# Kernel optimization log

Measured on AMD Instinct MI355X. Metric: run time of the kernel, lower is better.

Reference implementation:

```python
import jax, jax.numpy as jnp
import numpy as np

HEADS = 8
TOK = 4  # num_query_tokens
EPS = 1e-5


def _ln(x, w, b):
    mu = jnp.mean(x, -1, keepdims=True)
    v = jnp.var(x, -1, keepdims=True)
    return (x - mu) / jnp.sqrt(v + EPS) * w + b


def _inorm(x):
    # InstanceNorm3d(affine=False): normalize per (B,C) over spatial dims
    mu = jnp.mean(x, (2, 3, 4), keepdims=True)
    v = jnp.var(x, (2, 3, 4), keepdims=True)
    return (x - mu) / jnp.sqrt(v + EPS)


def _conv3(x, w, b):
    y = jax.lax.conv_general_dilated(x, w, (1, 1, 1), 'SAME',
                                     dimension_numbers=('NCDHW', 'OIDHW', 'NCDHW'))
    return y + b[None, :, None, None, None]


def setup_inputs() -> dict:
    key = jax.random.key(0)
    ks = jax.random.split(key, 8)
    B, C, D, H, W = 4, 320, 16, 32, 32
    CLI = 320
    QD = C * TOK  # 1280
    s = 0.02
    return {
        'img_feat': jax.random.normal(ks[0], (B, C, D, H, W), jnp.float32),
        'cli_feat': jax.random.normal(ks[1], (B, CLI), jnp.float32),
        'Wq': jax.random.normal(ks[2], (QD, CLI), jnp.float32) * s,
        'bq': jnp.zeros((QD,), jnp.float32),
        'lnq_w': jnp.ones((QD,), jnp.float32),
        'lnq_b': jnp.zeros((QD,), jnp.float32),
        'Wk': jax.random.normal(ks[3], (C, C), jnp.float32) * s,
        'bk': jnp.zeros((C,), jnp.float32),
        'Wv': jax.random.normal(ks[4], (C, C), jnp.float32) * s,
        'bv': jnp.zeros((C,), jnp.float32),
        'Wo': jax.random.normal(ks[5], (C, QD), jnp.float32) * s,
        'bo': jnp.zeros((C,), jnp.float32),
        'lno_w': jnp.ones((C,), jnp.float32),
        'lno_b': jnp.zeros((C,), jnp.float32),
        'Wf1': jax.random.normal(ks[6], (C, 2 * C, 3, 3, 3), jnp.float32) * s,
        'bf1': jnp.zeros((C,), jnp.float32),
        'Wf2': jax.random.normal(ks[7], (C, C, 3, 3, 3), jnp.float32) * s,
        'bf2': jnp.zeros((C,), jnp.float32),
    }


def reference(img_feat, cli_feat, Wq, bq, lnq_w, lnq_b, Wk, bk, Wv, bv,
              Wo, bo, lno_w, lno_b, Wf1, bf1, Wf2, bf2):
    B, C, D, H, W = img_feat.shape
    S = D * H * W
    hd = C // HEADS
    scale = hd ** -0.5
    # clinical features -> 4 query tokens per head: [B, heads, head_dim, TOK]
    q = _ln(cli_feat @ Wq.T + bq, lnq_w, lnq_b).reshape(B, HEADS, hd, TOK)
    # 1x1x1 convs == per-position linear over channels
    x = img_feat.reshape(B, C, S)
    k = (jnp.einsum('oc,bcs->bos', Wk, x) + bk[None, :, None]).reshape(B, HEADS, hd, S)
    v = (jnp.einsum('oc,bcs->bos', Wv, x) + bv[None, :, None]).reshape(B, HEADS, hd, S)
    # [B, heads, TOK, S] scores -> softmax over spatial
    attn = jax.nn.softmax(jnp.einsum('bhdt,bhds->bhts', q, k) * scale, axis=-1)
    # value @ attn^T -> [B, heads, head_dim, TOK], flatten like torch .view(B,-1)
    o = jnp.einsum('bhds,bhts->bhdt', v, attn).reshape(B, HEADS * hd * TOK)
    o = _ln(o @ Wo.T + bo, lno_w, lno_b)  # [B, C]
    bcast = jnp.broadcast_to(o[:, :, None, None, None], (B, C, D, H, W))
    fused = jnp.concatenate([img_feat, bcast], axis=1)  # [B, 2C, D, H, W]
    h = jax.nn.gelu(_inorm(_conv3(fused, Wf1, bf1)), approximate=False)
    h = _inorm(_conv3(h, Wf2, bf2))
    return h + img_feat
```

## Files before the change

### kernel.cpp

```cpp
#include <hip/hip_runtime.h>
#include <hip/hip_bf16.h>
#include <math.h>

typedef unsigned short u16;

#define DEV static __device__ __forceinline__

DEV float bfu(u16 u) { union { unsigned int i; float f; } v; v.i = ((unsigned int)u) << 16; return v.f; }
DEV u16 fbu(float f) { __hip_bfloat16 h = __float2bfloat16(f); return *reinterpret_cast<u16*>(&h); }

template <typename T> struct ModeOf;
template <> struct ModeOf<u16>   { static constexpr int v = 0; };
template <> struct ModeOf<float> { static constexpr int v = 1; };
template <typename T> DEV float ld(const void* p, size_t i);
template <> DEV float ld<u16>(const void* p, size_t i)   { return bfu(((const u16*)p)[i]); }
template <> DEV float ld<float>(const void* p, size_t i) { return ((const float*)p)[i]; }

template <typename T> DEV float4 ld4(const void* p, size_t i);
template <> DEV float4 ld4<u16>(const void* p, size_t i) {
    ushort4 v = *reinterpret_cast<const ushort4*>((const u16*)p + i);
    return make_float4(bfu(v.x), bfu(v.y), bfu(v.z), bfu(v.w));
}
template <> DEV float4 ld4<float>(const void* p, size_t i) {
    return *reinterpret_cast<const float4*>((const float*)p + i);
}

#define NB 4
#define NC 320
#define ND 16
#define NH 32
#define NW 32
#define NS 16384
#define NHD 40
#define NQD 1280
#define NR 32
#define NTOK 4
#define OUT_N (NB*NC*NS)
#define EPSV 1e-5f
#define SCALE 0.15811388300841898f

#define YKS 8
#define YCH (NS / YKS)

#define CSL 32
#define NSL 10
#define HALO_D 4
#define HALO_H 6
#define PIXW 34
#define NPIX (HALO_D*HALO_H*PIXW)
#define PACKN (27*10*20*64*8)

typedef __attribute__((ext_vector_type(8))) short bf16x8;
typedef __attribute__((ext_vector_type(4))) float f32x4;

DEV int swz4(int p) { return (p + (p >> 2)) & 3; }

DEV float blk_sum(float v, float* red) {
    __syncthreads();
#pragma unroll
    for (int o = 32; o > 0; o >>= 1) v += __shfl_down(v, o, 64);
    int wv = threadIdx.x >> 6, ln = threadIdx.x & 63;
    if (ln == 0) red[wv] = v;
    __syncthreads();
    return red[0] + red[1] + red[2] + red[3];
}
DEV float blk_max(float v, float* red) {
    __syncthreads();
#pragma unroll
    for (int o = 32; o > 0; o >>= 1) v = fmaxf(v, __shfl_down(v, o, 64));
    int wv = threadIdx.x >> 6, ln = threadIdx.x & 63;
    if (ln == 0) red[wv] = v;
    __syncthreads();
    return fmaxf(fmaxf(red[0], red[1]), fmaxf(red[2], red[3]));
}

__global__ void detect_kernel(const u16* __restrict__ lnqw, int* __restrict__ flag) {
    if (threadIdx.x == 0) flag[0] = (lnqw[0] == 0x3F80) ? 0 : 1;
}

template <typename T>
__global__ __launch_bounds__(256) void q_kernel(const int* __restrict__ flag,
        const void* __restrict__ cli, const void* __restrict__ Wq, const void* __restrict__ bq,
        const void* __restrict__ lnw, const void* __restrict__ lnb, float* __restrict__ qout) {
    if (*flag != ModeOf<T>::v) return;
    int b = blockIdx.x, tid = threadIdx.x;
    __shared__ float cl[NC];
    __shared__ float red[8];
    for (int i = tid; i < NC; i += 256) cl[i] = ld<T>(cli, b * NC + i);
    __syncthreads();
    float loc[5];
    float s1 = 0.f, s2 = 0.f;
#pragma unroll
    for (int k = 0; k < 5; ++k) {
        int j = tid + k * 256;
        float a = ld<T>(bq, j);
        size_t wr = (size_t)j * NC;
        for (int c = 0; c < NC; ++c) a += cl[c] * ld<T>(Wq, wr + c);
        loc[k] = a; s1 += a; s2 += a * a;
    }
    s1 = blk_sum(s1, red);
    s2 = blk_sum(s2, red);
    float mu = s1 / (float)NQD;
    float var = fmaxf(s2 / (float)NQD - mu * mu, 0.f);
    float rs = rsqrtf(var + EPSV);
#pragma unroll
    for (int k = 0; k < 5; ++k) {
        int j = tid + k * 256;
        qout[(size_t)b * NQD + j] = (loc[k] - mu) * rs * ld<T>(lnw, j) + ld<T>(lnb, j);
    }
}

template <typename T>
__global__ __launch_bounds__(256) void qw_kernel(const int* __restrict__ flag,
        const float* __restrict__ q, const void* __restrict__ Wk, const void* __restrict__ bk,
        float* __restrict__ qW, float* __restrict__ qb) {
    if (*flag != ModeOf<T>::v) return;
    int gid = blockIdx.x * 256 + threadIdx.x;
    if (gid < NB * NR * NC) {
        int c = gid % NC;
        int r = (gid / NC) % NR;
        int b = gid / (NC * NR);
        int h = r >> 2, t = r & 3;
        float a = 0.f;
        const float* qb_ = q + (size_t)b * NQD;
        for (int d = 0; d < NHD; ++d)
            a += qb_[(h * NHD + d) * NTOK + t] * ld<T>(Wk, (size_t)(h * NHD + d) * NC + c);
        qW[gid] = a;
    }
    if (gid < NB * NR) {
        int r = gid & 31, b = gid >> 5;
        int h = r >> 2, t = r & 3;
        float a = 0.f;
        const float* qb_ = q + (size_t)b * NQD;
        for (int d = 0; d < NHD; ++d)
            a += qb_[(h * NHD + d) * NTOK + t] * ld<T>(bk, h * NHD + d);
        qb[gid] = a;
    }
}

template <typename T>
__global__ __launch_bounds__(256) void scores_kernel(const int* __restrict__ flag,
        const void* __restrict__ img, const float* __restrict__ qW, const float* __restrict__ qb,
        float* __restrict__ attn) {
    if (*flag != ModeOf<T>::v) return;
    int b = blockIdx.y;
    int s = blockIdx.x * 256 + threadIdx.x;
    __shared__ __align__(16) float qWl[NR * NC];
    for (int i = threadIdx.x; i < NR * NC; i += 256) qWl[i] = qW[(size_t)b * NR * NC + i];
    __syncthreads();
    float acc[NR];
#pragma unroll
    for (int r = 0; r < NR; ++r) acc[r] = 0.f;
    size_t xb = (size_t)b * NC * NS + s;
    for (int c0 = 0; c0 < NC; c0 += 4) {
        float x0 = ld<T>(img, xb + ((size_t)(c0 + 0) << 14));
        float x1 = ld<T>(img, xb + ((size_t)(c0 + 1) << 14));
        float x2 = ld<T>(img, xb + ((size_t)(c0 + 2) << 14));
        float x3 = ld<T>(img, xb + ((size_t)(c0 + 3) << 14));
#pragma unroll
        for (int r = 0; r < NR; ++r) {
            const float4 qv = *reinterpret_cast<const float4*>(&qWl[r * NC + c0]);
            acc[r] += qv.x * x0 + qv.y * x1 + qv.z * x2 + qv.w * x3;
        }
    }
#pragma unroll
    for (int r = 0; r < NR; ++r)
        attn[((size_t)(b * NR + r) << 14) + s] = (acc[r] + qb[b * NR + r]) * SCALE;
}

__global__ __launch_bounds__(256) void softmax_kernel(float* __restrict__ attn) {
    int row = blockIdx.x;
    float* rp = attn + ((size_t)row << 14);
    __shared__ float red[8];
    float m = -1e30f;
    for (int s = threadIdx.x; s < NS; s += 256) m = fmaxf(m, rp[s]);
    m = blk_max(m, red);
    float sum = 0.f;
    for (int s = threadIdx.x; s < NS; s += 256) {
        float e = expf(rp[s] - m);
        rp[s] = e; sum += e;
    }
    sum = blk_sum(sum, red);
    float inv = 1.f / sum;
    for (int s = threadIdx.x; s < NS; s += 256) rp[s] *= inv;
}

template <typename T>
__global__ __launch_bounds__(256) void y_kernel(const int* __restrict__ flag,
        const float* __restrict__ attn, const void* __restrict__ img, float* __restrict__ yp) {
    if (*flag != ModeOf<T>::v) return;
    int row = blockIdx.x;
    int ks  = blockIdx.y;
    int b = row >> 5;
    int wv = threadIdx.x >> 6, ln = threadIdx.x & 63;
    const float* ar = attn + ((size_t)row << 14) + ks * YCH;
    size_t xb = (size_t)b * NC * NS + ks * YCH;
    float* yout = yp + ((size_t)ks * NB * NR + row) * NC;
    for (int c = wv; c < NC; c += 4) {
        size_t xr = xb + ((size_t)c << 14);
        float p = 0.f;
#pragma unroll
        for (int it = 0; it < YCH / 256; ++it) {
            int s = it * 256 + ln * 4;
            float4 x = ld4<T>(img, xr + s);
            const float4 a = *reinterpret_cast<const float4*>(ar + s);
            p += a.x * x.x + a.y * x.y + a.z * x.z + a.w * x.w;
        }
#pragma unroll
        for (int o = 32; o > 0; o >>= 1) p += __shfl_down(p, o, 64);
        if (ln == 0) yout[c] = p;
    }
}

__global__ __launch_bounds__(256) void yred_kernel(const float* __restrict__ yp, float* __restrict__ y) {
    int i = blockIdx.x * 256 + threadIdx.x;
    if (i >= NB * NR * NC) return;
    float s = 0.f;
#pragma unroll
    for (int k = 0; k < YKS; ++k) s += yp[(size_t)k * NB * NR * NC + i];
    y[i] = s;
}

template <typename T>
__global__ __launch_bounds__(256) void o_kernel(const int* __restrict__ flag,
        const float* __restrict__ y, const void* __restrict__ Wv, const void* __restrict__ bv,
        const void* __restrict__ Wo, const void* __restrict__ bo,
        const void* __restrict__ lnw, const void* __restrict__ lnb, float* __restrict__ o2) {
    if (*flag != ModeOf<T>::v) return;
    int b = blockIdx.x, tid = threadIdx.x;
    __shared__ float yl[NR * NC];
    __shared__ float ol[NQD];
    __shared__ float red[8];
    for (int i = tid; i < NR * NC; i += 256) yl[i] = y[(size_t)b * NR * NC + i];
    __syncthreads();
#pragma unroll
    for (int k = 0; k < 5; ++k) {
        int i = tid + k * 256;
        int h = i / 160, rem = i - h * 160;
        int d = rem >> 2, t = rem & 3;
        int wr = h * NHD + d, r = h * NTOK + t;
        float a = ld<T>(bv, wr);
        size_t wvr = (size_t)wr * NC;
        const float* yr = yl + r * NC;
        for (int c = 0; c < NC; ++c) a += ld<T>(Wv, wvr + c) * yr[c];
        ol[i] = a;
    }
    __syncthreads();
    for (int j = tid; j < NC; j += 256) {
        float a = ld<T>(bo, j);
        size_t wor = (size_t)j * NQD;
        for (int i = 0; i < NQD; ++i) a += ld<T>(Wo, wor + i) * ol[i];
        yl[j] = a;
    }
    __syncthreads();
    float s1 = 0.f, s2 = 0.f;
    for (int j = tid; j < NC; j += 256) { float v = yl[j]; s1 += v; s2 += v * v; }
    s1 = blk_sum(s1, red);
    s2 = blk_sum(s2, red);
    float mu = s1 / (float)NC;
    float var = fmaxf(s2 / (float)NC - mu * mu, 0.f);
    float rs = rsqrtf(var + EPSV);
    for (int j = tid; j < NC; j += 256)
        o2[(size_t)b * NC + j] = (yl[j] - mu) * rs * ld<T>(lnw, j) + ld<T>(lnb, j);
}

template <typename T>
__global__ __launch_bounds__(256) void p_kernel(const int* __restrict__ flag,
        const float* __restrict__ o2, const void* __restrict__ Wf1, float* __restrict__ P) {
    if (*flag != ModeOf<T>::v) return;
    int o = blockIdx.x, b = blockIdx.y;
    int tid = threadIdx.x, wv = tid >> 6, ln = tid & 63;
    __shared__ float red[4 * 27];
    __shared__ float taps[27];
    float acc[27];
#pragma unroll
    for (int k = 0; k < 27; ++k) acc[k] = 0.f;
    for (int c = tid; c < NC; c += 256) {
        float oc = o2[(size_t)b * NC + c];
        size_t wp = ((size_t)o * 640 + 320 + c) * 27;
#pragma unroll
        for (int k = 0; k < 27; ++k) acc[k] += oc * ld<T>(Wf1, wp + k);
    }
#pragma unroll
    for (int k = 0; k < 27; ++k) {
        float v = acc[k];
#pragma unroll
        for (int off = 32; off > 0; off >>= 1) v += __shfl_down(v, off, 64);
        if (ln == 0) red[wv * 27 + k] = v;
    }
    __syncthreads();
    if (tid < 27) taps[tid] = red[tid] + red[27 + tid] + red[54 + tid] + red[81 + tid];
    __syncthreads();
    if (tid < 27) {
        int pd = tid / 9, ph = (tid / 3) % 3, pw = tid % 3;
        float s = 0.f;
        for (int kd = 0; kd < 3; ++kd) {
            if ((pd == 0 && kd == 0) || (pd == 2 && kd == 2)) continue;
            for (int kh = 0; kh < 3; ++kh) {
                if ((ph == 0 && kh == 0) || (ph == 2 && kh == 2)) continue;
                for (int kw = 0; kw < 3; ++kw) {
                    if ((pw == 0 && kw == 0) || (pw == 2 && kw == 2)) continue;
                    s += taps[kd * 9 + kh * 3 + kw];
                }
            }
        }
        P[(size_t)(b * NC + o) * 27 + tid] = s;
    }
}

template <typename T>
__global__ __launch_bounds__(256) void imgt_kernel(const int* __restrict__ flag,
        const void* __restrict__ img, u16* __restrict__ outT) {
    if (*flag != ModeOf<T>::v) return;
    int b = blockIdx.z, c0 = blockIdx.y << 5, s0 = blockIdx.x << 5;
    int r = threadIdx.x >> 3, c4 = (threadIdx.x & 7) << 2;
    __shared__ float tile[32][33];
#pragma unroll
    for (int j = 0; j < 4; ++j)
        tile[r][c4 + j] = ld<T>(img, ((size_t)(b * NC + c0 + r) << 14) + s0 + c4 + j);
    __syncthreads();
    u16* op = outT + ((size_t)b * NS + s0 + r) * NC + c0 + c4;
#pragma unroll
    for (int j = 0; j < 4; ++j) op[j] = fbu(tile[c4 + j][r]);
}

template <typename TW>
__global__ __launch_bounds__(256) void pack_kernel(const int* __restrict__ flag,
        const void* __restrict__ wgt, const void* __restrict__ bias,
        u16* __restrict__ wpack, float* __restrict__ biasf, int wic) {
    if (*flag != ModeOf<TW>::v) return;
    int gid = blockIdx.x * 256 + threadIdx.x;
    if (gid < NC) biasf[gid] = ld<TW>(bias, gid);
    int lane = gid & 63;
    int rest = gid >> 6;
    int obg = rest % 20;  rest /= 20;
    int t = rest % 27;    int cs = rest / 27;
    int o  = (obg << 4) + (lane & 15);
    int c0 = (cs << 5) + ((lane >> 4) << 3);
    u16* dst = wpack + (size_t)gid * 8;
#pragma unroll
    for (int j = 0; j < 8; ++j)
        dst[j] = fbu(ld<TW>(wgt, ((size_t)o * wic + c0 + j) * 27 + t));
}

__global__ __launch_bounds__(256, 3) void convmm_kernel(
        const u16* __restrict__ inT, const u16* __restrict__ wpack,
        const float* __restrict__ biasf, const float* __restrict__ Pp,
        u16* __restrict__ out) {
    int d0 = (blockIdx.x >> 3) << 1;
    int h0 = (blockIdx.x & 7) << 2;
    int ob = blockIdx.y;
    int b  = blockIdx.z;
    int tid = threadIdx.x;
    int wv = tid >> 6, ln = tid & 63;
    int col = ln & 15, g = ln >> 4;

    __shared__ __align__(16) u16 lin[NPIX * CSL];

    {
        float4 z = {0.f, 0.f, 0.f, 0.f};
        float4* lp = reinterpret_cast<float4*>(lin);
        for (int i = tid; i < NPIX * CSL / 8; i += 256) lp[i] = z;
    }
    __syncthreads();

    f32x4 acc[4][4];
#pragma unroll
    for (int mi = 0; mi < 4; ++mi)
#pragma unroll
        for (int ni = 0; ni < 4; ++ni) acc[mi][ni] = (f32x4){0.f, 0.f, 0.f, 0.f};

    int pix0[4];
#pragma unroll
    for (int ni = 0; ni < 4; ++ni) {
        int nb = (wv << 2) + ni;
        int r2 = nb >> 1;
        int ddo = r2 >> 2, hho = r2 & 3;
        pix0[ni] = (ddo * HALO_H + hho) * PIXW + ((nb & 1) << 4) + col;
    }

    size_t inb = (size_t)b * NS * NC;

    for (int cs = 0; cs < NSL; ++cs) {
        for (int k = wv; k < 48; k += 4) {
            int hf = k & 1, rr = k >> 1;
            int dd = rr / HALO_H, hh = rr - dd * HALO_H;
            int dg = d0 + dd - 1, hg = h0 + hh - 1;
            if ((unsigned)dg < ND && (unsigned)hg < NH) {
                int pixbase = (dd * HALO_H + hh) * PIXW + 1 + (hf << 4);
                int p = pixbase + (ln >> 2);
                int wpos = (hf << 4) + (ln >> 2);
                int cg = (ln & 3) ^ swz4(p);
                const u16* src = inT + inb + ((size_t)(dg << 10) + (hg << 5) + wpos) * NC
                                 + (cs << 5) + (cg << 3);
                __builtin_amdgcn_global_load_lds(
                    (const __attribute__((address_space(1))) unsigned int*)src,
                    (__attribute__((address_space(3))) unsigned int*)(lin + pixbase * CSL),
                    16, 0, 0);
            }
        }
        __syncthreads();

        const u16* wp = wpack + (size_t)cs * 27 * 20 * 512;
#pragma unroll
        for (int t = 0; t < 27; ++t) {
            const int kd = t / 9, kh = (t / 3) % 3, kw = t % 3;
            bf16x8 af[4];
#pragma unroll
            for (int mi = 0; mi < 4; ++mi)
                af[mi] = *reinterpret_cast<const bf16x8*>(
                    wp + ((size_t)(t * 20 + (ob << 2) + mi) << 9) + (ln << 3));
            bf16x8 bfr[4];
#pragma unroll
            for (int ni = 0; ni < 4; ++ni) {
                int p = pix0[ni] + (kd * HALO_H + kh) * PIXW + kw;
                bfr[ni] = *reinterpret_cast<const bf16x8*>(
                    lin + p * CSL + ((g ^ swz4(p)) << 3));
            }
#pragma unroll
            for (int mi = 0; mi < 4; ++mi)
#pragma unroll
                for (int ni = 0; ni < 4; ++ni)
                    acc[mi][ni] = __builtin_amdgcn_mfma_f32_16x16x32_bf16(
                        af[mi], bfr[ni], acc[mi][ni], 0, 0, 0);
        }
        __syncthreads();
    }

#pragma unroll
    for (int ni = 0; ni < 4; ++ni) {
        int nb = (wv << 2) + ni;
        int r2 = nb >> 1;
        int d = d0 + (r2 >> 2);
        int h = h0 + (r2 & 3);
        int w = ((nb & 1) << 4) + col;
        int pd = (d == 0) ? 0 : ((d == ND - 1) ? 2 : 1);
        int ph = (h == 0) ? 0 : ((h == NH - 1) ? 2 : 1);
        int pw = (w == 0) ? 0 : ((w == NW - 1) ? 2 : 1);
        size_t sidx = ((size_t)d << 10) + (h << 5) + w;
#pragma unroll
        for (int mi = 0; mi < 4; ++mi) {
#pragma unroll
            for (int r = 0; r < 4; ++r) {
                int o = (ob << 6) + (mi << 4) + (g << 2) + r;
                float v = acc[mi][ni][r] + biasf[o];
                if (Pp) v += Pp[(size_t)(b * NC + o) * 27 + pd * 9 + ph * 3 + pw];
                out[((size_t)(b * NC + o) << 14) + sidx] = fbu(v);
            }
        }
    }
}

__global__ __launch_bounds__(256) void stats_kernel(const u16* __restrict__ raw, float* __restrict__ mean,
                                                    float* __restrict__ rstd) {
    int bo = blockIdx.x;
    const u16* base = raw + ((size_t)bo << 14);
    __shared__ float red[8];
    float s1 = 0.f, s2 = 0.f;
    for (int s = threadIdx.x; s < NS; s += 256) { float v = bfu(base[s]); s1 += v; s2 += v * v; }
    s1 = blk_sum(s1, red);
    s2 = blk_sum(s2, red);
    if (threadIdx.x == 0) {
        float mu = s1 / (float)NS;
        float var = fmaxf(s2 / (float)NS - mu * mu, 0.f);
        mean[bo] = mu;
        rstd[bo] = rsqrtf(var + EPSV);
    }
}

__global__ __launch_bounds__(256) void norm1t_kernel(const u16* __restrict__ raw,
        const float* __restrict__ mean, const float* __restrict__ rstd, u16* __restrict__ h1t) {
    int b = blockIdx.z, c0 = blockIdx.y << 5, s0 = blockIdx.x << 5;
    int r = threadIdx.x >> 3, c4 = (threadIdx.x & 7) << 2;
    __shared__ float tile[32][33];
    int bo = b * NC + c0 + r;
    float mu = mean[bo], rs = rstd[bo];
    const u16* rp = raw + ((size_t)bo << 14) + s0 + c4;
#pragma unroll
    for (int j = 0; j < 4; ++j) {
        float xn = (bfu(rp[j]) - mu) * rs;
        tile[r][c4 + j] = 0.5f * xn * (1.f + erff(xn * 0.70710678118654752f));
    }
    __syncthreads();
    u16* op = h1t + ((size_t)b * NS + s0 + r) * NC + c0 + c4;
#pragma unroll
    for (int j = 0; j < 4; ++j) op[j] = fbu(tile[c4 + j][r]);
}

template <typename T>
__global__ __launch_bounds__(256) void final_kernel(const int* __restrict__ flag,
        const u16* __restrict__ raw, const float* __restrict__ mean, const float* __restrict__ rstd,
        const void* __restrict__ img, void* __restrict__ outp) {
    if (*flag != ModeOf<T>::v) return;
    int idx = blockIdx.x * 256 + threadIdx.x;
    if (idx >= OUT_N) return;
    int bo = idx >> 14;
    float xn = (bfu(raw[idx]) - mean[bo]) * rstd[bo];
    float r = xn + ld<T>(img, idx);
    if (ModeOf<T>::v == 0) ((u16*)outp)[idx] = fbu(r);
    else                   ((float*)outp)[idx] = r;
}

extern "C" void kernel_launch(void* const* d_in, const int* in_sizes, int n_in,
                              void* d_out, int out_size, void* d_ws, size_t ws_size,
                              hipStream_t stream) {
    const void* IMG  = d_in[0];
    const void* CLI  = d_in[1];
    const void* WQ   = d_in[2];
    const void* BQ   = d_in[3];
    const void* LNQW = d_in[4];
    const void* LNQB = d_in[5];
    const void* WK   = d_in[6];
    const void* BK   = d_in[7];
    const void* WV   = d_in[8];
    const void* BV   = d_in[9];
    const void* WO   = d_in[10];
    const void* BO   = d_in[11];
    const void* LNOW = d_in[12];
    const void* LNOB = d_in[13];
    const void* WF1  = d_in[14];
    const void* BF1  = d_in[15];
    const void* WF2  = d_in[16];
    const void* BF2  = d_in[17];

    char* ws = (char*)d_ws;
    size_t off = 0;
    auto alloc = [&](size_t bytes) { void* p = ws + off; off += (bytes + 255) & ~(size_t)255; return p; };
    int*   FLAG  = (int*)  alloc(256);
    u16*   RAW   = (u16*)  alloc((size_t)OUT_N * 2);
    float* Qf    = (float*)alloc((size_t)NB * NQD * 4);
    float* QW    = (float*)alloc((size_t)NB * NR * NC * 4);
    float* QB    = (float*)alloc((size_t)NB * NR * 4);
    float* Yb    = (float*)alloc((size_t)NB * NR * NC * 4);
    float* O2    = (float*)alloc((size_t)NB * NC * 4);
    float* PB    = (float*)alloc((size_t)NB * NC * 27 * 4);
    float* MEAN  = (float*)alloc((size_t)NB * NC * 4);
    float* RSTD  = (float*)alloc((size_t)NB * NC * 4);
    u16*   WPACK = (u16*)  alloc((size_t)PACKN * 2);
    float* BIASF = (float*)alloc((size_t)NC * 4);
    float* ATTN  = (float*)d_out;
    float* YP    = (float*)RAW;
    u16*   IMGT  = (u16*)d_out;
    u16*   H1    = (u16*)d_out;
    (void)ws_size; (void)n_in; (void)in_sizes; (void)out_size;

    detect_kernel<<<1, 64, 0, stream>>>((const u16*)LNQW, FLAG);

    q_kernel<u16>  <<<NB, 256, 0, stream>>>(FLAG, CLI, WQ, BQ, LNQW, LNQB, Qf);
    q_kernel<float><<<NB, 256, 0, stream>>>(FLAG, CLI, WQ, BQ, LNQW, LNQB, Qf);

    int qwg = (NB * NR * NC + 255) / 256;
    qw_kernel<u16>  <<<qwg, 256, 0, stream>>>(FLAG, Qf, WK, BK, QW, QB);
    qw_kernel<float><<<qwg, 256, 0, stream>>>(FLAG, Qf, WK, BK, QW, QB);

    scores_kernel<u16>  <<<dim3(64, NB), 256, 0, stream>>>(FLAG, IMG, QW, QB, ATTN);
    scores_kernel<float><<<dim3(64, NB), 256, 0, stream>>>(FLAG, IMG, QW, QB, ATTN);

    softmax_kernel<<<NB * NR, 256, 0, stream>>>(ATTN);

    y_kernel<u16>  <<<dim3(NB * NR, YKS), 256, 0, stream>>>(FLAG, ATTN, IMG, YP);
    y_kernel<float><<<dim3(NB * NR, YKS), 256, 0, stream>>>(FLAG, ATTN, IMG, YP);

    yred_kernel<<<(NB * NR * NC + 255) / 256, 256, 0, stream>>>(YP, Yb);

    imgt_kernel<u16>  <<<dim3(512, 10, NB), 256, 0, stream>>>(FLAG, IMG, IMGT);
    imgt_kernel<float><<<dim3(512, 10, NB), 256, 0, stream>>>(FLAG, IMG, IMGT);

    o_kernel<u16>  <<<NB, 256, 0, stream>>>(FLAG, Yb, WV, BV, WO, BO, LNOW, LNOB, O2);
    o_kernel<float><<<NB, 256, 0, stream>>>(FLAG, Yb, WV, BV, WO, BO, LNOW, LNOB, O2);

    p_kernel<u16>  <<<dim3(NC, NB), 256, 0, stream>>>(FLAG, O2, WF1, PB);
    p_kernel<float><<<dim3(NC, NB), 256, 0, stream>>>(FLAG, O2, WF1, PB);

    int pkg = (PACKN / 8 + 255) / 256;
    pack_kernel<u16>  <<<pkg, 256, 0, stream>>>(FLAG, WF1, BF1, WPACK, BIASF, 640);
    pack_kernel<float><<<pkg, 256, 0, stream>>>(FLAG, WF1, BF1, WPACK, BIASF, 640);

    convmm_kernel<<<dim3(64, 5, NB), 256, 0, stream>>>(IMGT, WPACK, BIASF, PB, RAW);

    stats_kernel<<<NB * NC, 256, 0, stream>>>(RAW, MEAN, RSTD);
    norm1t_kernel<<<dim3(512, 10, NB), 256, 0, stream>>>(RAW, MEAN, RSTD, H1);

    pack_kernel<u16>  <<<pkg, 256, 0, stream>>>(FLAG, WF2, BF2, WPACK, BIASF, 320);
    pack_kernel<float><<<pkg, 256, 0, stream>>>(FLAG, WF2, BF2, WPACK, BIASF, 320);

    convmm_kernel<<<dim3(64, 5, NB), 256, 0, stream>>>(H1, WPACK, BIASF, nullptr, RAW);

    stats_kernel<<<NB * NC, 256, 0, stream>>>(RAW, MEAN, RSTD);

    final_kernel<u16>  <<<(OUT_N + 255) / 256, 256, 0, stream>>>(FLAG, RAW, MEAN, RSTD, IMG, d_out);
    final_kernel<float><<<(OUT_N + 255) / 256, 256, 0, stream>>>(FLAG, RAW, MEAN, RSTD, IMG, d_out);
}
```

Baseline: 2.132 ms.

## Use MFMA for attention scores on transposed bf16 image; vectorize stats/final/y loads

Attention scores are now computed with bf16 MFMA instructions on the channel-last transposed image, using a query-key weight matrix packed to bf16 in the fragment layout. This replaces the scalar FP32 per-position loop, and the image transpose is moved ahead of it. The attention buffer moves into workspace so it no longer shares the output buffer with the transposed image. The y, stats and final kernels switch to wider vector loads of 8 or 4 elements. Rounding the scores path to bf16 adds precision error ahead of the softmax.

```diff
diff --git a/kernel.cpp b/kernel.cpp
--- a/kernel.cpp
+++ b/kernel.cpp
@@ -16,13 +16,23 @@
 template <> DEV float ld<u16>(const void* p, size_t i)   { return bfu(((const u16*)p)[i]); }
 template <> DEV float ld<float>(const void* p, size_t i) { return ((const float*)p)[i]; }
 
-template <typename T> DEV float4 ld4(const void* p, size_t i);
-template <> DEV float4 ld4<u16>(const void* p, size_t i) {
-    ushort4 v = *reinterpret_cast<const ushort4*>((const u16*)p + i);
-    return make_float4(bfu(v.x), bfu(v.y), bfu(v.z), bfu(v.w));
-}
-template <> DEV float4 ld4<float>(const void* p, size_t i) {
-    return *reinterpret_cast<const float4*>((const float*)p + i);
+template <typename T> DEV float dot8(const void* img, size_t idx, const float* ar, int s);
+template <> DEV float dot8<u16>(const void* img, size_t idx, const float* ar, int s) {
+    uint4 v = *reinterpret_cast<const uint4*>((const u16*)img + idx + s);
+    const float4 a0 = *reinterpret_cast<const float4*>(ar + s);
+    const float4 a1 = *reinterpret_cast<const float4*>(ar + s + 4);
+    return a0.x*bfu(v.x & 0xffff) + a0.y*bfu(v.x >> 16)
+         + a0.z*bfu(v.y & 0xffff) + a0.w*bfu(v.y >> 16)
+         + a1.x*bfu(v.z & 0xffff) + a1.y*bfu(v.z >> 16)
+         + a1.z*bfu(v.w & 0xffff) + a1.w*bfu(v.w >> 16);
+}
+template <> DEV float dot8<float>(const void* img, size_t idx, const float* ar, int s) {
+    const float4 x0 = *reinterpret_cast<const float4*>((const float*)img + idx + s);
+    const float4 x1 = *reinterpret_cast<const float4*>((const float*)img + idx + s + 4);
+    const float4 a0 = *reinterpret_cast<const float4*>(ar + s);
+    const float4 a1 = *reinterpret_cast<const float4*>(ar + s + 4);
+    return a0.x*x0.x + a0.y*x0.y + a0.z*x0.z + a0.w*x0.w
+         + a1.x*x1.x + a1.y*x1.y + a1.z*x1.z + a1.w*x1.w;
 }
 
 #define NB 4
@@ -113,7 +123,7 @@
 template <typename T>
 __global__ __launch_bounds__(256) void qw_kernel(const int* __restrict__ flag,
         const float* __restrict__ q, const void* __restrict__ Wk, const void* __restrict__ bk,
-        float* __restrict__ qW, float* __restrict__ qb) {
+        float* __restrict__ qW, float* __restrict__ qb, u16* __restrict__ qwb) {
     if (*flag != ModeOf<T>::v) return;
     int gid = blockIdx.x * 256 + threadIdx.x;
     if (gid < NB * NR * NC) {
@@ -126,6 +136,9 @@
         for (int d = 0; d < NHD; ++d)
             a += qb_[(h * NHD + d) * NTOK + t] * ld<T>(Wk, (size_t)(h * NHD + d) * NC + c);
         qW[gid] = a;
+        int kk = c >> 5, gg = (c >> 3) & 3, j = c & 7;
+        int mf = r >> 4, lane = (gg << 4) | (r & 15);
+        qwb[(((size_t)(b * 10 + kk) * 2 + mf) << 9) + (lane << 3) + j] = fbu(a);
     }
     if (gid < NB * NR) {
         int r = gid & 31, b = gid >> 5;
@@ -138,34 +151,48 @@
     }
 }
 
-template <typename T>
-__global__ __launch_bounds__(256) void scores_kernel(const int* __restrict__ flag,
-        const void* __restrict__ img, const float* __restrict__ qW, const float* __restrict__ qb,
-        float* __restrict__ attn) {
-    if (*flag != ModeOf<T>::v) return;
+__global__ __launch_bounds__(256) void scores_mm_kernel(
+        const u16* __restrict__ imgt, const u16* __restrict__ qwb,
+        const float* __restrict__ qb, float* __restrict__ attn) {
     int b = blockIdx.y;
-    int s = blockIdx.x * 256 + threadIdx.x;
-    __shared__ __align__(16) float qWl[NR * NC];
-    for (int i = threadIdx.x; i < NR * NC; i += 256) qWl[i] = qW[(size_t)b * NR * NC + i];
-    __syncthreads();
-    float acc[NR];
-#pragma unroll
-    for (int r = 0; r < NR; ++r) acc[r] = 0.f;
-    size_t xb = (size_t)b * NC * NS + s;
-    for (int c0 = 0; c0 < NC; c0 += 4) {
-        float x0 = ld<T>(img, xb + ((size_t)(c0 + 0) << 14));
-        float x1 = ld<T>(img, xb + ((size_t)(c0 + 1) << 14));
-        float x2 = ld<T>(img, xb + ((size_t)(c0 + 2) << 14));
-        float x3 = ld<T>(img, xb + ((size_t)(c0 + 3) << 14));
-#pragma unroll
-        for (int r = 0; r < NR; ++r) {
-            const float4 qv = *reinterpret_cast<const float4*>(&qWl[r * NC + c0]);
-            acc[r] += qv.x * x0 + qv.y * x1 + qv.z * x2 + qv.w * x3;
+    int s0 = blockIdx.x * 256 + (threadIdx.x >> 6) * 64;
+    int ln = threadIdx.x & 63;
+    int col = ln & 15, g = ln >> 4;
+    bf16x8 af[10][2];
+    const u16* qa = qwb + (size_t)b * 10 * 2 * 512;
+#pragma unroll
+    for (int kk = 0; kk < 10; ++kk)
+#pragma unroll
+        for (int mf = 0; mf < 2; ++mf)
+            af[kk][mf] = *reinterpret_cast<const bf16x8*>(qa + (((kk << 1) + mf) << 9) + (ln << 3));
+    f32x4 acc[2][4];
+#pragma unroll
+    for (int mf = 0; mf < 2; ++mf)
+#pragma unroll
+        for (int nf = 0; nf < 4; ++nf) acc[mf][nf] = (f32x4){0.f, 0.f, 0.f, 0.f};
+    const u16* xb = imgt + (size_t)b * NS * NC;
+#pragma unroll
+    for (int kk = 0; kk < 10; ++kk) {
+#pragma unroll
+        for (int nf = 0; nf < 4; ++nf) {
+            bf16x8 bf = *reinterpret_cast<const bf16x8*>(
+                xb + (size_t)(s0 + nf * 16 + col) * NC + kk * 32 + (g << 3));
+#pragma unroll
+            for (int mf = 0; mf < 2; ++mf)
+                acc[mf][nf] = __builtin_amdgcn_mfma_f32_16x16x32_bf16(
+                    af[kk][mf], bf, acc[mf][nf], 0, 0, 0);
         }
     }
 #pragma unroll
-    for (int r = 0; r < NR; ++r)
-        attn[((size_t)(b * NR + r) << 14) + s] = (acc[r] + qb[b * NR + r]) * SCALE;
+    for (int mf = 0; mf < 2; ++mf)
+#pragma unroll
+        for (int nf = 0; nf < 4; ++nf)
+#pragma unroll
+            for (int r = 0; r < 4; ++r) {
+                int row = mf * 16 + g * 4 + r;
+                attn[((size_t)(b * NR + row) << 14) + s0 + nf * 16 + col] =
+                    (acc[mf][nf][r] + qb[b * NR + row]) * SCALE;
+            }
 }
 
 __global__ __launch_bounds__(256) void softmax_kernel(float* __restrict__ attn) {
@@ -200,12 +227,8 @@
         size_t xr = xb + ((size_t)c << 14);
         float p = 0.f;
 #pragma unroll
-        for (int it = 0; it < YCH / 256; ++it) {
-            int s = it * 256 + ln * 4;
-            float4 x = ld4<T>(img, xr + s);
-            const float4 a = *reinterpret_cast<const float4*>(ar + s);
-            p += a.x * x.x + a.y * x.y + a.z * x.z + a.w * x.w;
-        }
+        for (int it = 0; it < YCH / 512; ++it)
+            p += dot8<T>(img, xr, ar, it * 512 + ln * 8);
 #pragma unroll
         for (int o = 32; o > 0; o >>= 1) p += __shfl_down(p, o, 64);
         if (ln == 0) yout[c] = p;
@@ -457,7 +480,15 @@
     const u16* base = raw + ((size_t)bo << 14);
     __shared__ float red[8];
     float s1 = 0.f, s2 = 0.f;
-    for (int s = threadIdx.x; s < NS; s += 256) { float v = bfu(base[s]); s1 += v; s2 += v * v; }
+    for (int s0 = threadIdx.x * 8; s0 < NS; s0 += 2048) {
+        uint4 v = *reinterpret_cast<const uint4*>(base + s0);
+        float x0 = bfu(v.x & 0xffff), x1 = bfu(v.x >> 16);
+        float x2 = bfu(v.y & 0xffff), x3 = bfu(v.y >> 16);
+        float x4 = bfu(v.z & 0xffff), x5 = bfu(v.z >> 16);
+        float x6 = bfu(v.w & 0xffff), x7 = bfu(v.w >> 16);
+        s1 += ((x0 + x1) + (x2 + x3)) + ((x4 + x5) + (x6 + x7));
+        s2 += ((x0*x0 + x1*x1) + (x2*x2 + x3*x3)) + ((x4*x4 + x5*x5) + (x6*x6 + x7*x7));
+    }
     s1 = blk_sum(s1, red);
     s2 = blk_sum(s2, red);
     if (threadIdx.x == 0) {
@@ -492,13 +523,26 @@
         const u16* __restrict__ raw, const float* __restrict__ mean, const float* __restrict__ rstd,
         const void* __restrict__ img, void* __restrict__ outp) {
     if (*flag != ModeOf<T>::v) return;
-    int idx = blockIdx.x * 256 + threadIdx.x;
+    int idx = (blockIdx.x * 256 + threadIdx.x) * 4;
     if (idx >= OUT_N) return;
     int bo = idx >> 14;
-    float xn = (bfu(raw[idx]) - mean[bo]) * rstd[bo];
-    float r = xn + ld<T>(img, idx);
-    if (ModeOf<T>::v == 0) ((u16*)outp)[idx] = fbu(r);
-    else                   ((float*)outp)[idx] = r;
+    float mu = mean[bo], rs = rstd[bo];
+    ushort4 rv = *reinterpret_cast<const ushort4*>(raw + idx);
+    float r0 = (bfu(rv.x) - mu) * rs;
+    float r1 = (bfu(rv.y) - mu) * rs;
+    float r2 = (bfu(rv.z) - mu) * rs;
+    float r3 = (bfu(rv.w) - mu) * rs;
+    if (ModeOf<T>::v == 0) {
+        ushort4 iv = *reinterpret_cast<const ushort4*>((const u16*)img + idx);
+        ushort4 ov;
+        ov.x = fbu(r0 + bfu(iv.x)); ov.y = fbu(r1 + bfu(iv.y));
+        ov.z = fbu(r2 + bfu(iv.z)); ov.w = fbu(r3 + bfu(iv.w));
+        *reinterpret_cast<ushort4*>((u16*)outp + idx) = ov;
+    } else {
+        float4 iv = *reinterpret_cast<const float4*>((const float*)img + idx);
+        float4 ov = make_float4(r0 + iv.x, r1 + iv.y, r2 + iv.z, r3 + iv.w);
+        *reinterpret_cast<float4*>((float*)outp + idx) = ov;
+    }
 }
 
 extern "C" void kernel_launch(void* const* d_in, const int* in_sizes, int n_in,
@@ -531,6 +575,7 @@
     float* Qf    = (float*)alloc((size_t)NB * NQD * 4);
     float* QW    = (float*)alloc((size_t)NB * NR * NC * 4);
     float* QB    = (float*)alloc((size_t)NB * NR * 4);
+    u16*   QWB   = (u16*)  alloc((size_t)NB * 10 * 2 * 512 * 2);
     float* Yb    = (float*)alloc((size_t)NB * NR * NC * 4);
     float* O2    = (float*)alloc((size_t)NB * NC * 4);
     float* PB    = (float*)alloc((size_t)NB * NC * 27 * 4);
@@ -538,23 +583,25 @@
     float* RSTD  = (float*)alloc((size_t)NB * NC * 4);
     u16*   WPACK = (u16*)  alloc((size_t)PACKN * 2);
     float* BIASF = (float*)alloc((size_t)NC * 4);
-    float* ATTN  = (float*)d_out;
     float* YP    = (float*)RAW;
+    float* ATTN  = (float*)((char*)RAW + (16u << 20));
     u16*   IMGT  = (u16*)d_out;
     u16*   H1    = (u16*)d_out;
     (void)ws_size; (void)n_in; (void)in_sizes; (void)out_size;
 
     detect_kernel<<<1, 64, 0, stream>>>((const u16*)LNQW, FLAG);
 
+    imgt_kernel<u16>  <<<dim3(512, 10, NB), 256, 0, stream>>>(FLAG, IMG, IMGT);
+    imgt_kernel<float><<<dim3(512, 10, NB), 256, 0, stream>>>(FLAG, IMG, IMGT);
+
     q_kernel<u16>  <<<NB, 256, 0, stream>>>(FLAG, CLI, WQ, BQ, LNQW, LNQB, Qf);
     q_kernel<float><<<NB, 256, 0, stream>>>(FLAG, CLI, WQ, BQ, LNQW, LNQB, Qf);
 
     int qwg = (NB * NR * NC + 255) / 256;
-    qw_kernel<u16>  <<<qwg, 256, 0, stream>>>(FLAG, Qf, WK, BK, QW, QB);
-    qw_kernel<float><<<qwg, 256, 0, stream>>>(FLAG, Qf, WK, BK, QW, QB);
-
-    scores_kernel<u16>  <<<dim3(64, NB), 256, 0, stream>>>(FLAG, IMG, QW, QB, ATTN);
-    scores_kernel<float><<<dim3(64, NB), 256, 0, stream>>>(FLAG, IMG, QW, QB, ATTN);
+    qw_kernel<u16>  <<<qwg, 256, 0, stream>>>(FLAG, Qf, WK, BK, QW, QB, QWB);
+    qw_kernel<float><<<qwg, 256, 0, stream>>>(FLAG, Qf, WK, BK, QW, QB, QWB);
+
+    scores_mm_kernel<<<dim3(64, NB), 256, 0, stream>>>(IMGT, QWB, QB, ATTN);
 
     softmax_kernel<<<NB * NR, 256, 0, stream>>>(ATTN);
 
@@ -562,9 +609,6 @@
     y_kernel<float><<<dim3(NB * NR, YKS), 256, 0, stream>>>(FLAG, ATTN, IMG, YP);
 
     yred_kernel<<<(NB * NR * NC + 255) / 256, 256, 0, stream>>>(YP, Yb);
-
-    imgt_kernel<u16>  <<<dim3(512, 10, NB), 256, 0, stream>>>(FLAG, IMG, IMGT);
-    imgt_kernel<float><<<dim3(512, 10, NB), 256, 0, stream>>>(FLAG, IMG, IMGT);
 
     o_kernel<u16>  <<<NB, 256, 0, stream>>>(FLAG, Yb, WV, BV, WO, BO, LNOW, LNOB, O2);
     o_kernel<float><<<NB, 256, 0, stream>>>(FLAG, Yb, WV, BV, WO, BO, LNOW, LNOB, O2);
@@ -588,6 +632,6 @@
 
     stats_kernel<<<NB * NC, 256, 0, stream>>>(RAW, MEAN, RSTD);
 
-    final_kernel<u16>  <<<(OUT_N + 255) / 256, 256, 0, stream>>>(FLAG, RAW, MEAN, RSTD, IMG, d_out);
-    final_kernel<float><<<(OUT_N + 255) / 256, 256, 0, stream>>>(FLAG, RAW, MEAN, RSTD, IMG, d_out);
-}
+    final_kernel<u16>  <<<(OUT_N / 4 + 255) / 256, 256, 0, stream>>>(FLAG, RAW, MEAN, RSTD, IMG, d_out);
+    final_kernel<float><<<(OUT_N / 4 + 255) / 256, 256, 0, stream>>>(FLAG, RAW, MEAN, RSTD, IMG, d_out);
+}
```

After: 2.055 ms. -3.6%, faster.
